# Kernel optimization log

Hardware: AMD Instinct MI355X
Metric: run time of the kernel (lower is better)

Reference implementation:

```python
import jax, jax.numpy as jnp
import numpy as np
from jax import lax

NH = 1024
CATS = 1024
B = 64
T = 512


def setup_inputs() -> dict:
    key = jax.random.key(0)
    ks = jax.random.split(key, 12)
    s_in = 1.0 / np.sqrt(CATS)
    s_h = 1.0 / np.sqrt(NH)
    return {
        "x": jax.random.normal(ks[0], (B, T, CATS), jnp.float32),
        "h0": jax.random.normal(ks[1], (B, NH), jnp.float32),
        # torch Linear weights are [out, in]
        "Wh": jax.random.uniform(ks[2], (NH, CATS), jnp.float32, -s_in, s_in),
        "Wz": jax.random.uniform(ks[3], (NH, CATS), jnp.float32, -s_in, s_in),
        "Wr": jax.random.uniform(ks[4], (NH, CATS), jnp.float32, -s_in, s_in),
        "Uh": jax.random.uniform(ks[5], (NH, NH), jnp.float32, -s_h, s_h),
        "Uz": jax.random.uniform(ks[6], (NH, NH), jnp.float32, -s_h, s_h),
        "Ur": jax.random.uniform(ks[7], (NH, NH), jnp.float32, -s_h, s_h),
        "bz": jax.random.uniform(ks[8], (NH,), jnp.float32, -s_h, s_h),
        "br": jax.random.uniform(ks[9], (NH,), jnp.float32, -s_h, s_h),
        "Wout": jax.random.uniform(ks[10], (CATS, NH), jnp.float32, -s_h, s_h),
    }


def _gru_last_h(x, h0, Wh, Wz, Wr, Uh, Uz, Ur, bz, br):
    # Precompute input projections as big GEMMs: [B,T,nh] each
    xh = jnp.einsum('btc,hc->bth', x, Wh)
    xz = jnp.einsum('btc,hc->bth', x, Wz)
    # Note: reset gate r is computed in the original but NEVER used in htilde
    # (htilde = tanh(Wh x + Uh h)); it does not affect the output, so we omit it.
    # Scan over time: inputs as [T, B, nh]
    seq = (jnp.swapaxes(xh, 0, 1), jnp.swapaxes(xz, 0, 1))

    def step(h, inp):
        xh_t, xz_t = inp
        z = jax.nn.sigmoid(xz_t + h @ Uz.T + bz)
        htilde = jnp.tanh(xh_t + h @ Uh.T)
        h_new = (1.0 - z) * h + z * htilde
        return h_new, None

    hT, _ = lax.scan(step, h0, seq)
    return hT  # [B, nh]


def reference(x, h0, Wh, Wz, Wr, Uh, Uz, Ur, bz, br, Wout):
    hT = _gru_last_h(x, h0, Wh, Wz, Wr, Uh, Uz, Ur, bz, br)
    return hT @ Wout.T  # [B, cats]
```

## Files before the change

### kernel.cpp

```cpp
#include <hip/hip_runtime.h>

typedef __attribute__((ext_vector_type(8))) short short8v;
typedef __attribute__((ext_vector_type(4))) float f32x4;
typedef __attribute__((ext_vector_type(4))) float float4v;
typedef unsigned long long u64;

#define NHID 1024
#define NCAT 1024
#define NB   64
#define NT   512
#define RING_STRIDE 65536

__device__ __forceinline__ short f2bf(float f) {
  union { float f; unsigned u; } c; c.f = f;
  unsigned r = (c.u + 0x7fffu + ((c.u >> 16) & 1u)) >> 16;
  return (short)r;
}

__device__ __forceinline__ void ast(u64* p, u64 v) {
  __hip_atomic_store(p, v, __ATOMIC_RELAXED, __HIP_MEMORY_SCOPE_AGENT);
}

__device__ __forceinline__ short8v cvt8(float4v a, float4v b) {
  short8v s;
  s[0]=f2bf(a[0]); s[1]=f2bf(a[1]); s[2]=f2bf(a[2]); s[3]=f2bf(a[3]);
  s[4]=f2bf(b[0]); s[5]=f2bf(b[1]); s[6]=f2bf(b[2]); s[7]=f2bf(b[3]);
  return s;
}

__global__ __launch_bounds__(256, 1) void gru_kernel(
    const float* __restrict__ h0, const float* __restrict__ Wh, const float* __restrict__ Wz,
    const float* __restrict__ Uh, const float* __restrict__ Uz, const float* __restrict__ bz,
    const float* __restrict__ Wout, const float* __restrict__ x,
    short* __restrict__ ring, unsigned* __restrict__ flags, float* __restrict__ out)
{
  extern __shared__ char smem[];
  short8v* ufr = (short8v*)smem;
  float*   red = (float*)(smem + 131072);
  short*   rp  = (short*)(smem + 131072 + 12288);

  __builtin_amdgcn_fence(__ATOMIC_ACQUIRE, "agent");

  const int tid  = threadIdx.x;
  const int lane = tid & 63;
  const int wv   = tid >> 6;
  const int mt   = blockIdx.x >> 6;
  const int cg   = blockIdx.x & 63;
  const int col  = lane & 15;
  const int quad = lane >> 4;
  const int kq   = quad * 8;
  const int jg   = cg * 16 + col;

  for (int idx = tid; idx < 64 * 2 * 64; idx += 256) {
    int l  = idx & 63;
    int nt = (idx >> 6) & 1;
    int kb = idx >> 7;
    int j  = cg * 16 + (l & 15);
    int k0 = (kb & 31) * 32 + (l >> 4) * 8;
    const float* M = (kb < 32) ? (nt ? Uh : Uz) : (nt ? Wh : Wz);
    short8v v;
#pragma unroll
    for (int e = 0; e < 8; ++e) v[e] = f2bf(M[j * 1024 + k0 + e]);
    ufr[idx] = v;
  }
  __syncthreads();

  float hl[4] = {0.f, 0.f, 0.f, 0.f};
  float bzv = 0.f;
  if (wv == 0) {
    bzv = bz[jg];
#pragma unroll
    for (int r = 0; r < 4; ++r) hl[r] = h0[(mt * 16 + quad * 4 + r) * NHID + jg];
  }

  const int kb0 = wv * 16;
  unsigned* myflag = flags + (mt * 64 + cg) * 16;
  const unsigned* pollp  = flags + (mt * 64 + (wv & 1) * 32 + (lane & 31)) * 16;
  const unsigned* pollpt = flags + (mt * 64 + wv * 16 + (lane & 15)) * 16;

  short8v xf[16];
  if (wv >= 2) {
    const float* xrow = x + ((long)(mt * 16 + col) * NT + 0) * NCAT + (kb0 - 32) * 32 + kq;
#pragma unroll
    for (int i = 0; i < 16; ++i)
      xf[i] = cvt8(*(const float4v*)(xrow + i * 32), *(const float4v*)(xrow + i * 32 + 4));
  }

  for (int t = 0; t < NT; ++t) {
    const int par = t & 1;
    f32x4 pz = {0.f,0.f,0.f,0.f}, ph = {0.f,0.f,0.f,0.f};

    if (wv < 2) {
      short8v f[16];
      if (t > 0) {
        const unsigned tt = (unsigned)t;
        for (;;) {
          unsigned v = __hip_atomic_load(pollp, __ATOMIC_RELAXED, __HIP_MEMORY_SCOPE_AGENT);
          if (__ballot(v < tt) == 0ull) break;
          __builtin_amdgcn_s_sleep(1);
        }
        __asm__ volatile("" ::: "memory");
        const short* hrow = ring + (size_t)t * RING_STRIDE
                          + (mt * 16 + col) * 1024 + kb0 * 32 + kq;
#pragma unroll
        for (int i = 0; i < 16; ++i) f[i] = *(const short8v*)(hrow + i * 32);
      } else {
        const float* hrow = h0 + (mt * 16 + col) * NHID + kb0 * 32 + kq;
#pragma unroll
        for (int i = 0; i < 16; ++i)
          f[i] = cvt8(*(const float4v*)(hrow + i * 32), *(const float4v*)(hrow + i * 32 + 4));
      }
#pragma unroll
      for (int i = 0; i < 16; ++i) {
        int kb = kb0 + i;
        pz = __builtin_amdgcn_mfma_f32_16x16x32_bf16(f[i], ufr[kb * 128 + lane],      pz, 0, 0, 0);
        ph = __builtin_amdgcn_mfma_f32_16x16x32_bf16(f[i], ufr[kb * 128 + 64 + lane], ph, 0, 0, 0);
      }
    } else {
#pragma unroll
      for (int i = 0; i < 16; ++i) {
        int kb = kb0 + i;
        pz = __builtin_amdgcn_mfma_f32_16x16x32_bf16(xf[i], ufr[kb * 128 + lane],      pz, 0, 0, 0);
        ph = __builtin_amdgcn_mfma_f32_16x16x32_bf16(xf[i], ufr[kb * 128 + 64 + lane], ph, 0, 0, 0);
      }
      if (t + 1 < NT) {
        const float* xrow = x + ((long)(mt * 16 + col) * NT + (t + 1)) * NCAT + (kb0 - 32) * 32 + kq;
#pragma unroll
        for (int i = 0; i < 16; ++i)
          xf[i] = cvt8(*(const float4v*)(xrow + i * 32), *(const float4v*)(xrow + i * 32 + 4));
      }
    }

    if (wv != 0) {
      float* sl = red + ((par * 3 + (wv - 1)) * 64 + lane) * 8;
      *(f32x4*)sl       = pz;
      *(f32x4*)(sl + 4) = ph;
    }
    __syncthreads();

    if (wv == 0) {
      f32x4 accz = pz, acch = ph;
#pragma unroll
      for (int s = 0; s < 3; ++s) {
        const float* sl = red + ((par * 3 + s) * 64 + lane) * 8;
        accz += *(const f32x4*)sl;
        acch += *(const f32x4*)(sl + 4);
      }
#pragma unroll
      for (int r = 0; r < 4; ++r) {
        float zp = accz[r] + bzv;
        float z  = 1.f / (1.f + __expf(-zp));
        float ht = 2.f / (1.f + __expf(-2.f * acch[r])) - 1.f;
        float v  = hl[r] + z * (ht - hl[r]);
        hl[r] = v;
        rp[(quad * 4 + r) * 16 + col] = f2bf(v);
      }
      __asm__ volatile("s_waitcnt lgkmcnt(0)" ::: "memory");
      u64 val = ((const u64*)rp)[lane];
      u64* hnq = (u64*)(ring + (size_t)(t + 1) * RING_STRIDE);
      ast(hnq + (mt * 16 + (lane >> 2)) * 256 + cg * 4 + (lane & 3), val);
      __asm__ volatile("s_waitcnt vmcnt(0)" ::: "memory");
      if (lane == 0)
        __hip_atomic_store(myflag, (unsigned)(t + 1), __ATOMIC_RELAXED, __HIP_MEMORY_SCOPE_AGENT);
    }
  }

  {
    for (;;) {
      unsigned v = __hip_atomic_load(pollpt, __ATOMIC_RELAXED, __HIP_MEMORY_SCOPE_AGENT);
      if (__ballot(v < (unsigned)NT) == 0ull) break;
      __builtin_amdgcn_s_sleep(1);
    }
    __asm__ volatile("" ::: "memory");
    const int kb0t = wv * 8;
    const short* hrow = ring + (size_t)NT * RING_STRIDE
                      + (mt * 16 + col) * 1024 + kb0t * 32 + kq;
    f32x4 acc = {0.f,0.f,0.f,0.f};
    const float* wrow = Wout + (long)jg * NHID + kb0t * 32 + kq;
#pragma unroll
    for (int kb = 0; kb < 8; ++kb) {
      short8v a = *(const short8v*)(hrow + kb * 32);
      float4v w0 = *(const float4v*)(wrow + kb * 32);
      float4v w1 = *(const float4v*)(wrow + kb * 32 + 4);
      acc = __builtin_amdgcn_mfma_f32_16x16x32_bf16(a, cvt8(w0, w1), acc, 0, 0, 0);
    }
    if (wv != 0)
      *(f32x4*)(red + ((wv - 1) * 64 + lane) * 8) = acc;
    __syncthreads();
    if (wv == 0) {
#pragma unroll
      for (int s = 0; s < 3; ++s)
        acc += *(const f32x4*)(red + (s * 64 + lane) * 8);
#pragma unroll
      for (int r = 0; r < 4; ++r)
        out[(mt * 16 + quad * 4 + r) * NCAT + jg] = acc[r];
    }
  }
}

extern "C" void kernel_launch(void* const* d_in, const int* in_sizes, int n_in,
                              void* d_out, int out_size, void* d_ws, size_t ws_size,
                              hipStream_t stream) {
  const float* x    = (const float*)d_in[0];
  const float* h0   = (const float*)d_in[1];
  const float* Wh   = (const float*)d_in[2];
  const float* Wz   = (const float*)d_in[3];
  const float* Uh   = (const float*)d_in[5];
  const float* Uz   = (const float*)d_in[6];
  const float* bz   = (const float*)d_in[8];
  const float* Wout = (const float*)d_in[10];

  char* ws = (char*)d_ws;
  unsigned* flags = (unsigned*)ws;
  short* ring = (short*)(ws + 16384);

  hipMemsetAsync(flags, 0, 16384, stream);

  hipFuncSetAttribute((const void*)gru_kernel,
                      hipFuncAttributeMaxDynamicSharedMemorySize, 143872);
  gru_kernel<<<256, 256, 143872, stream>>>(h0, Wh, Wz, Uh, Uz, bz, Wout, x,
                                           ring, flags, (float*)d_out);
}
```

Before: 2.409 ms.

## Replace per-block step flags with sentinel-valued ring data polling

```diff
diff --git a/kernel.cpp b/kernel.cpp
--- a/kernel.cpp
+++ b/kernel.cpp
@@ -4,12 +4,14 @@
 typedef __attribute__((ext_vector_type(4))) float f32x4;
 typedef __attribute__((ext_vector_type(4))) float float4v;
 typedef unsigned long long u64;
+typedef unsigned int u32;
 
 #define NHID 1024
 #define NCAT 1024
 #define NB   64
 #define NT   512
-#define RING_STRIDE 65536
+#define RINGQ 16384
+#define SENT32 0xFFFFFFFFu
 
 __device__ __forceinline__ short f2bf(float f) {
   union { float f; unsigned u; } c; c.f = f;
@@ -19,6 +21,9 @@
 
 __device__ __forceinline__ void ast(u64* p, u64 v) {
   __hip_atomic_store(p, v, __ATOMIC_RELAXED, __HIP_MEMORY_SCOPE_AGENT);
+}
+__device__ __forceinline__ u64 ald(const u64* p) {
+  return __hip_atomic_load((u64*)p, __ATOMIC_RELAXED, __HIP_MEMORY_SCOPE_AGENT);
 }
 
 __device__ __forceinline__ short8v cvt8(float4v a, float4v b) {
@@ -32,12 +37,12 @@
     const float* __restrict__ h0, const float* __restrict__ Wh, const float* __restrict__ Wz,
     const float* __restrict__ Uh, const float* __restrict__ Uz, const float* __restrict__ bz,
     const float* __restrict__ Wout, const float* __restrict__ x,
-    short* __restrict__ ring, unsigned* __restrict__ flags, float* __restrict__ out)
+    u64* __restrict__ ring, float* __restrict__ out)
 {
   extern __shared__ char smem[];
   short8v* ufr = (short8v*)smem;
   float*   red = (float*)(smem + 131072);
-  short*   rp  = (short*)(smem + 131072 + 12288);
+  short*   rp  = (short*)(smem + 131072 + 16384);
 
   __builtin_amdgcn_fence(__ATOMIC_ACQUIRE, "agent");
 
@@ -65,22 +70,13 @@
   }
   __syncthreads();
 
-  float hl[4] = {0.f, 0.f, 0.f, 0.f};
-  float bzv = 0.f;
-  if (wv == 0) {
-    bzv = bz[jg];
-#pragma unroll
-    for (int r = 0; r < 4; ++r) hl[r] = h0[(mt * 16 + quad * 4 + r) * NHID + jg];
-  }
-
+  float hl = h0[(mt * 16 + quad * 4 + wv) * NHID + jg];
+  const float bzv = bz[jg];
   const int kb0 = wv * 16;
-  unsigned* myflag = flags + (mt * 64 + cg) * 16;
-  const unsigned* pollp  = flags + (mt * 64 + (wv & 1) * 32 + (lane & 31)) * 16;
-  const unsigned* pollpt = flags + (mt * 64 + wv * 16 + (lane & 15)) * 16;
 
   short8v xf[16];
   if (wv >= 2) {
-    const float* xrow = x + ((long)(mt * 16 + col) * NT + 0) * NCAT + (kb0 - 32) * 32 + kq;
+    const float* xrow = x + ((long)(mt * 16 + col) * NT) * NCAT + (kb0 - 32) * 32 + kq;
 #pragma unroll
     for (int i = 0; i < 16; ++i)
       xf[i] = cvt8(*(const float4v*)(xrow + i * 32), *(const float4v*)(xrow + i * 32 + 4));
@@ -93,17 +89,24 @@
     if (wv < 2) {
       short8v f[16];
       if (t > 0) {
-        const unsigned tt = (unsigned)t;
+        const u64* hp = ring + (size_t)t * RINGQ + (mt * 16 + col) * 256 + kb0 * 8 + quad * 2;
+        u64 d[32];
         for (;;) {
-          unsigned v = __hip_atomic_load(pollp, __ATOMIC_RELAXED, __HIP_MEMORY_SCOPE_AGENT);
-          if (__ballot(v < tt) == 0ull) break;
+          bool ok = true;
+#pragma unroll
+          for (int i = 0; i < 16; ++i) { d[2*i] = ald(hp + i*8); d[2*i+1] = ald(hp + i*8 + 1); }
+#pragma unroll
+          for (int i = 0; i < 32; ++i)
+            ok &= ((u32)d[i] != SENT32) & ((u32)(d[i] >> 32) != SENT32);
+          if (__ballot(!ok) == 0ull) break;
           __builtin_amdgcn_s_sleep(1);
         }
-        __asm__ volatile("" ::: "memory");
-        const short* hrow = ring + (size_t)t * RING_STRIDE
-                          + (mt * 16 + col) * 1024 + kb0 * 32 + kq;
-#pragma unroll
-        for (int i = 0; i < 16; ++i) f[i] = *(const short8v*)(hrow + i * 32);
+#pragma unroll
+        for (int i = 0; i < 16; ++i) {
+          union { u64 u[2]; short8v v; } un;
+          un.u[0] = d[2*i]; un.u[1] = d[2*i+1];
+          f[i] = un.v;
+        }
       } else {
         const float* hrow = h0 + (mt * 16 + col) * NHID + kb0 * 32 + kq;
 #pragma unroll
@@ -131,69 +134,72 @@
       }
     }
 
-    if (wv != 0) {
-      float* sl = red + ((par * 3 + (wv - 1)) * 64 + lane) * 8;
-      *(f32x4*)sl       = pz;
-      *(f32x4*)(sl + 4) = ph;
+    {
+      float* base = red + ((par * 4 + wv) * 8) * 64 + lane;
+#pragma unroll
+      for (int c = 0; c < 4; ++c) { base[c * 64] = pz[c]; base[(4 + c) * 64] = ph[c]; }
     }
     __syncthreads();
 
-    if (wv == 0) {
-      f32x4 accz = pz, acch = ph;
-#pragma unroll
-      for (int s = 0; s < 3; ++s) {
-        const float* sl = red + ((par * 3 + s) * 64 + lane) * 8;
-        accz += *(const f32x4*)sl;
-        acch += *(const f32x4*)(sl + 4);
-      }
-#pragma unroll
-      for (int r = 0; r < 4; ++r) {
-        float zp = accz[r] + bzv;
-        float z  = 1.f / (1.f + __expf(-zp));
-        float ht = 2.f / (1.f + __expf(-2.f * acch[r])) - 1.f;
-        float v  = hl[r] + z * (ht - hl[r]);
-        hl[r] = v;
-        rp[(quad * 4 + r) * 16 + col] = f2bf(v);
-      }
+    {
+      float az = 0.f, ah = 0.f;
+#pragma unroll
+      for (int s = 0; s < 4; ++s) {
+        az += red[((par * 4 + s) * 8 + wv) * 64 + lane];
+        ah += red[((par * 4 + s) * 8 + 4 + wv) * 64 + lane];
+      }
+      float z  = 1.f / (1.f + __expf(-(az + bzv)));
+      float ht = 2.f / (1.f + __expf(-2.f * ah)) - 1.f;
+      float v  = hl + z * (ht - hl);
+      hl = v;
+      rp[wv * 64 + quad * 16 + col] = f2bf(v);
       __asm__ volatile("s_waitcnt lgkmcnt(0)" ::: "memory");
-      u64 val = ((const u64*)rp)[lane];
-      u64* hnq = (u64*)(ring + (size_t)(t + 1) * RING_STRIDE);
-      ast(hnq + (mt * 16 + (lane >> 2)) * 256 + cg * 4 + (lane & 3), val);
-      __asm__ volatile("s_waitcnt vmcnt(0)" ::: "memory");
-      if (lane == 0)
-        __hip_atomic_store(myflag, (unsigned)(t + 1), __ATOMIC_RELAXED, __HIP_MEMORY_SCOPE_AGENT);
+      if (lane < 16) {
+        u64 val = ((const u64*)rp)[wv * 16 + lane];
+        int rowg = mt * 16 + (lane >> 2) * 4 + wv;
+        ast(ring + (size_t)(t + 1) * RINGQ + rowg * 256 + cg * 4 + (lane & 3), val);
+      }
     }
   }
 
   {
+    const int kb0t = wv * 8;
+    const u64* hp = ring + (size_t)NT * RINGQ + (mt * 16 + col) * 256 + kb0t * 8 + quad * 2;
+    u64 d[16];
     for (;;) {
-      unsigned v = __hip_atomic_load(pollpt, __ATOMIC_RELAXED, __HIP_MEMORY_SCOPE_AGENT);
-      if (__ballot(v < (unsigned)NT) == 0ull) break;
+      bool ok = true;
+#pragma unroll
+      for (int i = 0; i < 8; ++i) { d[2*i] = ald(hp + i*8); d[2*i+1] = ald(hp + i*8 + 1); }
+#pragma unroll
+      for (int i = 0; i < 16; ++i)
+        ok &= ((u32)d[i] != SENT32) & ((u32)(d[i] >> 32) != SENT32);
+      if (__ballot(!ok) == 0ull) break;
       __builtin_amdgcn_s_sleep(1);
     }
-    __asm__ volatile("" ::: "memory");
-    const int kb0t = wv * 8;
-    const short* hrow = ring + (size_t)NT * RING_STRIDE
-                      + (mt * 16 + col) * 1024 + kb0t * 32 + kq;
     f32x4 acc = {0.f,0.f,0.f,0.f};
     const float* wrow = Wout + (long)jg * NHID + kb0t * 32 + kq;
 #pragma unroll
     for (int kb = 0; kb < 8; ++kb) {
-      short8v a = *(const short8v*)(hrow + kb * 32);
+      union { u64 u[2]; short8v v; } un;
+      un.u[0] = d[2*kb]; un.u[1] = d[2*kb+1];
       float4v w0 = *(const float4v*)(wrow + kb * 32);
       float4v w1 = *(const float4v*)(wrow + kb * 32 + 4);
-      acc = __builtin_amdgcn_mfma_f32_16x16x32_bf16(a, cvt8(w0, w1), acc, 0, 0, 0);
-    }
-    if (wv != 0)
-      *(f32x4*)(red + ((wv - 1) * 64 + lane) * 8) = acc;
+      acc = __builtin_amdgcn_mfma_f32_16x16x32_bf16(un.v, cvt8(w0, w1), acc, 0, 0, 0);
+    }
+    {
+      float* base = red + (wv * 8) * 64 + lane;
+#pragma unroll
+      for (int c = 0; c < 4; ++c) base[c * 64] = acc[c];
+    }
     __syncthreads();
     if (wv == 0) {
 #pragma unroll
-      for (int s = 0; s < 3; ++s)
-        acc += *(const f32x4*)(red + (s * 64 + lane) * 8);
-#pragma unroll
-      for (int r = 0; r < 4; ++r)
-        out[(mt * 16 + quad * 4 + r) * NCAT + jg] = acc[r];
+      for (int r = 0; r < 4; ++r) {
+        float a = 0.f;
+#pragma unroll
+        for (int s = 0; s < 4; ++s) a += red[(s * 8 + r) * 64 + lane];
+        out[(mt * 16 + quad * 4 + r) * NCAT + jg] = a;
+      }
     }
   }
 }
@@ -210,14 +216,11 @@
   const float* bz   = (const float*)d_in[8];
   const float* Wout = (const float*)d_in[10];
 
-  char* ws = (char*)d_ws;
-  unsigned* flags = (unsigned*)ws;
-  short* ring = (short*)(ws + 16384);
-
-  hipMemsetAsync(flags, 0, 16384, stream);
+  u64* ring = (u64*)d_ws;
+  hipMemsetAsync(ring, 0xFF, (size_t)513 * 131072, stream);
 
   hipFuncSetAttribute((const void*)gru_kernel,
-                      hipFuncAttributeMaxDynamicSharedMemorySize, 143872);
-  gru_kernel<<<256, 256, 143872, stream>>>(h0, Wh, Wz, Uh, Uz, bz, Wout, x,
-                                           ring, flags, (float*)d_out);
-}
+                      hipFuncAttributeMaxDynamicSharedMemorySize, 147968);
+  gru_kernel<<<256, 256, 147968, stream>>>(h0, Wh, Wz, Uh, Uz, bz, Wout, x,
+                                           ring, (float*)d_out);
+}
```

Result: slower. 3.678 ms (+52.6%).
